# Kernel tuning notes

Hardware: AMD Instinct MI355X
Metric: run time of the kernel (lower is better)

## Reference

```python
import jax, jax.numpy as jnp
import numpy as np

B, N, D, H = 8, 2048, 256, 4
HD = D // H


def setup_inputs() -> dict:
    key = jax.random.key(0)
    ks = jax.random.split(key, 12)
    s = 1.0 / np.sqrt(D)
    inp = {
        "node_features": jax.random.normal(ks[0], (B, N, D), dtype=jnp.float32),
        "causal_mask": jnp.tril(jnp.ones((N, N), dtype=jnp.float32)),
        "Wq": jax.random.normal(ks[1], (D, D), dtype=jnp.float32) * s,
        "bq": jnp.zeros((D,), dtype=jnp.float32),
        "Wk": jax.random.normal(ks[2], (D, D), dtype=jnp.float32) * s,
        "bk": jnp.zeros((D,), dtype=jnp.float32),
        "Wv": jax.random.normal(ks[3], (D, D), dtype=jnp.float32) * s,
        "bv": jnp.zeros((D,), dtype=jnp.float32),
        "Wo": jax.random.normal(ks[4], (D, D), dtype=jnp.float32) * s,
        "bo": jnp.zeros((D,), dtype=jnp.float32),
        "Wu": jax.random.normal(ks[5], (2 * D, D), dtype=jnp.float32) * (1.0 / np.sqrt(2 * D)),
        "bu": jnp.zeros((D,), dtype=jnp.float32),
    }
    return inp


def reference(node_features, causal_mask, Wq, bq, Wk, bk, Wv, bv, Wo, bo, Wu, bu):
    # node_features: [B, N, D]; causal_mask: [N, N] (1 = keep, 0 = masked)
    x = node_features
    # project and split heads -> [B, H, N, HD]
    def heads(w, b):
        return (x @ w + b).reshape(B, N, H, HD).transpose(0, 2, 1, 3)
    q, k, v = heads(Wq, bq), heads(Wk, bk), heads(Wv, bv)
    scale = 1.0 / np.sqrt(HD).astype(np.float32)
    scores = jnp.einsum("bhnd,bhmd->bhnm", q, k) * scale  # [B, H, N, N]
    scores = jnp.where(causal_mask > 0, scores, jnp.float32(-1e9))
    attn = jax.nn.softmax(scores, axis=-1)
    ctx = jnp.einsum("bhnm,bhmd->bhnd", attn, v)  # [B, H, N, HD]
    messages = ctx.transpose(0, 2, 1, 3).reshape(B, N, D) @ Wo + bo  # [B, N, D]
    combined = jnp.concatenate([x, messages], axis=-1)  # [B, N, 2D]
    updated = jax.nn.relu(combined @ Wu + bu)  # [B, N, D]  (dropout = identity in eval)
    return updated
```

## Files before the change

kernel.cpp:

```cpp
#include <hip/hip_runtime.h>
#include <math.h>

constexpr int B  = 8;
constexpr int N  = 2048;
constexpr int D  = 256;
constexpr int H  = 4;
constexpr int HD = 64;
constexpr int MTOT = B * N;

typedef __attribute__((ext_vector_type(8))) short  short8;
typedef __attribute__((ext_vector_type(4))) float  floatx4;
typedef unsigned short ushort_t;

#define QSCALE 0.1803368801111204f

__device__ __forceinline__ unsigned short f2bf(float f) {
    unsigned u = __float_as_uint(f);
    u += 0x7fffu + ((u >> 16) & 1u);
    return (unsigned short)(u >> 16);
}

__device__ __forceinline__ unsigned short f2bf_t(float f) {
    return (unsigned short)(__float_as_uint(f) >> 16);
}

__device__ __forceinline__ void gl_lds16(const ushort_t* g, ushort_t* l) {
    __builtin_amdgcn_global_load_lds(
        (const __attribute__((address_space(1))) void*)g,
        (__attribute__((address_space(3))) void*)l, 16, 0, 0);
}

__global__ __launch_bounds__(256) void prep(
    const float* __restrict__ x,
    const float* __restrict__ Wq, const float* __restrict__ Wk,
    const float* __restrict__ Wv, const float* __restrict__ Wo,
    const float* __restrict__ Wu,
    ushort_t* __restrict__ xb,
    ushort_t* __restrict__ wqkvt, ushort_t* __restrict__ wut,
    ushort_t* __restrict__ wbt,   ushort_t* __restrict__ wob)
{
    __shared__ float Ls[64][65];
    const int bx = blockIdx.x;
    const int t  = threadIdx.x;

    if (bx < 2048) {
        int idx = (bx * 256 + t) * 8;
        float4 a = *(const float4*)(x + idx);
        float4 b = *(const float4*)(x + idx + 4);
        ushort_t o[8] = {f2bf(a.x), f2bf(a.y), f2bf(a.z), f2bf(a.w),
                         f2bf(b.x), f2bf(b.y), f2bf(b.z), f2bf(b.w)};
        *(short8*)(xb + idx) = *(const short8*)o;
        return;
    }

    if (bx < 2112) {
        const int e  = bx - 2048;
        const int zz = e >> 4;
        const int kt = (e >> 2) & 3;
        const int nt = e & 3;
        const float* src; ushort_t* dst; int K;
        if      (zz == 0) { src = Wq; dst = wqkvt;          K = 256; }
        else if (zz == 1) { src = Wk; dst = wqkvt + 65536;  K = 256; }
        else if (zz == 2) { src = Wv; dst = wqkvt + 131072; K = 256; }
        else              { src = Wu; dst = wut;            K = 512; }
        #pragma unroll
        for (int i = 0; i < 16; i++) {
            int ee = t + i * 256, r = ee >> 6, c = ee & 63;
            Ls[r][c] = src[(size_t)(kt * 64 + r) * 256 + nt * 64 + c];
        }
        __syncthreads();
        #pragma unroll
        for (int i = 0; i < 16; i++) {
            int ee = t + i * 256, r = ee >> 6, c = ee & 63;
            dst[(size_t)(nt * 64 + r) * K + kt * 64 + c] = f2bf(Ls[c][r]);
        }
        return;
    }

    if (bx < 2128) {
        const int e  = bx - 2112;
        const int kt = e >> 2;
        const int nt = e & 3;
        #pragma unroll
        for (int i = 0; i < 16; i++) {
            int ee = t + i * 256, r = ee >> 6, c = ee & 63;
            Ls[r][c] = Wu[(size_t)(256 + kt * 64 + r) * 256 + nt * 64 + c];
        }
        __syncthreads();
        #pragma unroll
        for (int i = 0; i < 16; i++) {
            int ee = t + i * 256, r = ee >> 6, c = ee & 63;
            wbt[(size_t)(nt * 64 + r) * 256 + kt * 64 + c] = f2bf(Ls[c][r]);
        }
        return;
    }

    {
        int idx = ((bx - 2128) * 256 + t) * 8;
        float4 a = *(const float4*)(Wo + idx);
        float4 b = *(const float4*)(Wo + idx + 4);
        ushort_t o[8] = {f2bf(a.x), f2bf(a.y), f2bf(a.z), f2bf(a.w),
                         f2bf(b.x), f2bf(b.y), f2bf(b.z), f2bf(b.w)};
        *(short8*)(wob + idx) = *(const short8*)o;
    }
}

__global__ __launch_bounds__(256) void qkv_gemm(
    const ushort_t* __restrict__ xb, const ushort_t* __restrict__ wqkvt,
    const ushort_t* __restrict__ wob, const ushort_t* __restrict__ wbt,
    const float* __restrict__ Wu,
    const float* __restrict__ bq, const float* __restrict__ bk,
    const float* __restrict__ bv, const float* __restrict__ bo,
    const float* __restrict__ bu,
    ushort_t* __restrict__ q, ushort_t* __restrict__ kout,
    ushort_t* __restrict__ vt,
    ushort_t* __restrict__ wut, float* __restrict__ b2)
{
    __shared__ ushort_t SH[16896];
    ushort_t* As = SH;
    ushort_t* Bs = SH + 8192;

    const int t = threadIdx.x, w = t >> 6, lane = t & 63;
    const int quad = lane >> 4, l16 = lane & 15;
    const int bx = blockIdx.x;
    const int wr = (w >> 1) * 64, wc = (w & 1) * 64;

    if (blockIdx.y == 128) {
        if (bx < 4) {
            const int row0 = (bx >> 1) * 128;
            const int col0 = (bx & 1) * 128;
            floatx4 acc[4][4] = {};
            for (int k0 = 0; k0 < 256; k0 += 64) {
                __syncthreads();
                #pragma unroll
                for (int i = 0; i < 4; i++) {
                    int e = t + (i << 8);
                    int r = e >> 3, c8 = (e & 7) << 3;
                    gl_lds16(wob + (size_t)(row0 + r) * 256 + k0 + c8, &As[e * 8]);
                    gl_lds16(wbt + (size_t)(col0 + r) * 256 + k0 + c8, &Bs[e * 8]);
                }
                __syncthreads();
                #pragma unroll
                for (int kk = 0; kk < 64; kk += 32) {
                    short8 af[4], bf[4];
                    #pragma unroll
                    for (int i = 0; i < 4; i++)
                        af[i] = *(const short8*)&As[(wr + i * 16 + l16) * 64 + kk + quad * 8];
                    #pragma unroll
                    for (int j = 0; j < 4; j++)
                        bf[j] = *(const short8*)&Bs[(wc + j * 16 + l16) * 64 + kk + quad * 8];
                    #pragma unroll
                    for (int i = 0; i < 4; i++)
                        #pragma unroll
                        for (int j = 0; j < 4; j++)
                            acc[i][j] = __builtin_amdgcn_mfma_f32_16x16x32_bf16(
                                af[i], bf[j], acc[i][j], 0, 0, 0);
                }
            }
            #pragma unroll
            for (int j = 0; j < 4; j++) {
                int cl = wc + j * 16 + l16;
                #pragma unroll
                for (int i = 0; i < 4; i++)
                    #pragma unroll
                    for (int r = 0; r < 4; r++) {
                        int ml = wr + i * 16 + quad * 4 + r;
                        wut[(size_t)(col0 + cl) * 512 + 256 + row0 + ml] =
                            f2bf(acc[i][j][r]);
                    }
            }
        } else if (bx == 4) {
            float s0 = 0.f, s1 = 0.f, s2 = 0.f, s3 = 0.f;
            for (int j = 0; j < 64; j++) {
                s0 = fmaf(bo[j],       Wu[(size_t)(256 + j)       * 256 + t], s0);
                s1 = fmaf(bo[j + 64],  Wu[(size_t)(256 + j + 64)  * 256 + t], s1);
                s2 = fmaf(bo[j + 128], Wu[(size_t)(256 + j + 128) * 256 + t], s2);
                s3 = fmaf(bo[j + 192], Wu[(size_t)(256 + j + 192) * 256 + t], s3);
            }
            b2[t] = bu[t] + ((s0 + s1) + (s2 + s3));
        }
        return;
    }

    const int col0 = bx * 128, row0 = blockIdx.y * 128;

    floatx4 acc[4][4] = {};

    for (int k0 = 0; k0 < 256; k0 += 64) {
        __syncthreads();
        #pragma unroll
        for (int i = 0; i < 4; i++) {
            int e = t + (i << 8);
            int r = e >> 3, c8 = (e & 7) << 3;
            gl_lds16(xb    + (size_t)(row0 + r) * 256 + k0 + c8, &As[e * 8]);
            gl_lds16(wqkvt + (size_t)(col0 + r) * 256 + k0 + c8, &Bs[e * 8]);
        }
        __syncthreads();

        #pragma unroll
        for (int kk = 0; kk < 64; kk += 32) {
            short8 af[4], bf[4];
            #pragma unroll
            for (int i = 0; i < 4; i++)
                af[i] = *(const short8*)&As[(wr + i * 16 + l16) * 64 + kk + quad * 8];
            #pragma unroll
            for (int j = 0; j < 4; j++)
                bf[j] = *(const short8*)&Bs[(wc + j * 16 + l16) * 64 + kk + quad * 8];
            #pragma unroll
            for (int i = 0; i < 4; i++)
                #pragma unroll
                for (int j = 0; j < 4; j++)
                    acc[i][j] = __builtin_amdgcn_mfma_f32_16x16x32_bf16(
                        af[i], bf[j], acc[i][j], 0, 0, 0);
        }
    }

    const int kind = bx >> 1;
    const float* bias = (kind == 0) ? bq : (kind == 1 ? bk : bv);
    const float scl  = (kind == 0) ? QSCALE : 1.0f;
    __syncthreads();
    ushort_t (*Ts)[132] = (ushort_t(*)[132])SH;
    #pragma unroll
    for (int j = 0; j < 4; j++) {
        int cl = wc + j * 16 + l16;
        float bsv = bias[(bx & 1) * 128 + cl];
        #pragma unroll
        for (int i = 0; i < 4; i++) {
            #pragma unroll
            for (int r = 0; r < 4; r++) {
                int ml = wr + i * 16 + quad * 4 + r;
                ushort_t bvv = f2bf((acc[i][j][r] + bsv) * scl);
                if (kind < 2) Ts[ml][cl] = bvv;
                else          Ts[cl][ml] = bvv;
            }
        }
    }
    __syncthreads();

    const int b = row0 >> 11, n0 = row0 & (N - 1);
    #pragma unroll
    for (int i = 0; i < 8; i++) {
        int id = t + (i << 8);
        int rr = id >> 4, c8 = (id & 15) << 3;
        short8 val = *(const short8*)&Ts[rr][c8];
        if (kind < 2) {
            int cg = (bx & 1) * 128 + c8;
            int h = cg >> 6, hd = cg & 63;
            if (kind == 0) {
                *(short8*)&q[(((size_t)(b * H + h)) * N + n0 + rr) * HD + hd] = val;
            } else {
                int hd2 = (((hd >> 3) ^ (rr & 7)) << 3);
                *(short8*)&kout[(((size_t)(b * H + h)) * N + n0 + rr) * HD + hd2] = val;
            }
        } else {
            int cg = (bx & 1) * 128 + rr;
            int h = cg >> 6, hd = cg & 63;
            int u  = id & 15;
            int up = (u & 8) | ((u ^ hd) & 7);
            *(short8*)&vt[(((size_t)(b * H + h)) * HD + hd) * N + n0 + (up << 3)] = val;
        }
    }
}

__global__ __launch_bounds__(512) void attn_mfma(
    const ushort_t* __restrict__ q,
    const ushort_t* __restrict__ k,
    const ushort_t* __restrict__ vt,
    ushort_t* __restrict__ ctxb)
{
    __shared__ ushort_t Ks [2][128 * 64];
    __shared__ ushort_t Vts[2][64 * 128];
    __shared__ ushort_t Ps [8][16][36];

    const int t    = threadIdx.x;
    const int w    = t >> 6;
    const int lane = t & 63;
    const int quad = lane >> 4;
    const int l16  = lane & 15;
    const int swz  = l16 & 7;
    const int bh   = blockIdx.x;
    const int b    = bh >> 2, h = bh & 3;
    const int by   = blockIdx.y;
    const int grp  = w >> 2;
    const int qt   = grp ? by : (31 - by);
    const int qbase = qt * 64;
    const int rowb  = qbase + (w & 3) * 16;

    const ushort_t* qp = q  + (size_t)bh * N * HD;
    const ushort_t* kp = k  + (size_t)bh * N * HD;
    const ushort_t* vp = vt + (size_t)bh * HD * N;

    short8 qf0, qf1;
    {
        const ushort_t* qrow = qp + (size_t)(rowb + l16) * HD + quad * 8;
        qf0 = *(const short8*)(qrow);
        qf1 = *(const short8*)(qrow + 32);
    }

    floatx4 acc_o[4] = {};
    float plsum[4] = {};

    const int nkt_self = (qt >> 1) + 1;
    const int nkt_max  = ((31 - by) >> 1) + 1;

    #pragma unroll
    for (int i = 0; i < 2; i++) {
        int e = t + (i << 9);
        gl_lds16(kp + (((size_t)(e >> 3)) << 6) + ((e & 7) << 3),
                 &Ks[0][e * 8]);
        gl_lds16(vp + (size_t)(e >> 4) * N + ((e & 15) << 3),
                 &Vts[0][e * 8]);
    }
    __syncthreads();

    for (int kt = 0; kt < nkt_max; kt++) {
        const int kbase = kt * 128;
        const int cur   = kt & 1;

        if (kt + 1 < nkt_max) {
            const int kb2 = kbase + 128;
            #pragma unroll
            for (int i = 0; i < 2; i++) {
                int e = t + (i << 9);
                gl_lds16(kp + (((size_t)(kb2 + (e >> 3))) << 6) + ((e & 7) << 3),
                         &Ks[cur ^ 1][e * 8]);
                gl_lds16(vp + (size_t)(e >> 4) * N + kb2 + ((e & 15) << 3),
                         &Vts[cur ^ 1][e * 8]);
            }
        }

        if (kt < nkt_self) {
            const ushort_t* Ksc  = Ks[cur];
            const ushort_t* Vtsc = Vts[cur];

            int rem = rowb + 15 - kbase;
            int nch = (rem < 0) ? 0 : ((rem >> 5) + 1);
            if (nch > 4) nch = 4;

            for (int ch = 0; ch < nch; ch++) {
                #pragma unroll
                for (int c2 = 0; c2 < 2; c2++) {
                    const int ct = ch * 2 + c2;
                    const int krow = (ct * 16 + l16) * 64;
                    short8 kf0 = *(const short8*)&Ksc[krow + ((quad ^ swz) << 3)];
                    short8 kf1 = *(const short8*)&Ksc[krow + (((4 + quad) ^ swz) << 3)];
                    floatx4 z = {0.0f, 0.0f, 0.0f, 0.0f};
                    __builtin_amdgcn_s_setprio(1);
                    floatx4 s = __builtin_amdgcn_mfma_f32_16x16x32_bf16(qf0, kf0, z, 0, 0, 0);
                    s         = __builtin_amdgcn_mfma_f32_16x16x32_bf16(qf1, kf1, s, 0, 0, 0);
                    __builtin_amdgcn_s_setprio(0);
                    const bool partial = (kbase + ct * 16 + 15) > rowb;
                    if (partial) {
                        const int keyg = kbase + ct * 16 + l16;
                        #pragma unroll
                        for (int r = 0; r < 4; r++) {
                            float sv = s[r];
                            if (keyg > rowb + quad * 4 + r) sv = -3.0e38f;
                            float pv = __builtin_amdgcn_exp2f(sv);
                            plsum[r] += pv;
                            Ps[w][quad * 4 + r][c2 * 16 + l16] = f2bf_t(pv);
                        }
                    } else {
                        #pragma unroll
                        for (int r = 0; r < 4; r++) {
                            float pv = __builtin_amdgcn_exp2f(s[r]);
                            plsum[r] += pv;
                            Ps[w][quad * 4 + r][c2 * 16 + l16] = f2bf_t(pv);
                        }
                    }
                }
                short8 pf = *(const short8*)&Ps[w][l16][quad * 8];
                const int uu = ch * 4 + quad;
                const int up = (uu & 8) | ((uu ^ l16) & 7);
                __builtin_amdgcn_s_setprio(1);
                #pragma unroll
                for (int nt = 0; nt < 4; nt++) {
                    short8 vf = *(const short8*)&Vtsc[(nt * 16 + l16) * 128 + (up << 3)];
                    acc_o[nt] = __builtin_amdgcn_mfma_f32_16x16x32_bf16(pf, vf, acc_o[nt], 0, 0, 0);
                }
                __builtin_amdgcn_s_setprio(0);
            }
        }

        __syncthreads();
    }

    #pragma unroll
    for (int r = 0; r < 4; r++) {
        float l = plsum[r];
        l += __shfl_xor(l, 1);
        l += __shfl_xor(l, 2);
        l += __shfl_xor(l, 4);
        l += __shfl_xor(l, 8);
        float inv = 1.0f / l;
        int   n   = rowb + quad * 4 + r;
        #pragma unroll
        for (int nt = 0; nt < 4; nt++) {
            ctxb[((size_t)(b * N + n)) * D + h * HD + nt * 16 + l16] =
                f2bf(acc_o[nt][r] * inv);
        }
    }
}

__global__ __launch_bounds__(256) void tail2(
    const ushort_t* __restrict__ xb, const ushort_t* __restrict__ ctxb,
    const ushort_t* __restrict__ wut, const float* __restrict__ b2,
    float* __restrict__ out)
{
    __shared__ ushort_t As[64 * 64];
    __shared__ ushort_t Bs[128 * 64];

    const int t = threadIdx.x, w = t >> 6, lane = t & 63;
    const int quad = lane >> 4, l16 = lane & 15;
    const int col0 = blockIdx.x * 128, row0 = blockIdx.y * 64;
    const int wr = (w >> 1) * 32, wc = (w & 1) * 64;

    floatx4 acc[2][4] = {};

    for (int k0 = 0; k0 < 512; k0 += 64) {
        const ushort_t* Ab = (k0 < 256) ? xb : ctxb;
        const int ka = k0 & 255;
        __syncthreads();
        #pragma unroll
        for (int i = 0; i < 2; i++) {
            int e = t + (i << 8);
            int r = e >> 3, c8 = (e & 7) << 3;
            gl_lds16(Ab + (size_t)(row0 + r) * 256 + ka + c8, &As[e * 8]);
        }
        #pragma unroll
        for (int i = 0; i < 4; i++) {
            int e = t + (i << 8);
            int r = e >> 3, c8 = (e & 7) << 3;
            gl_lds16(wut + (size_t)(col0 + r) * 512 + k0 + c8, &Bs[e * 8]);
        }
        __syncthreads();

        #pragma unroll
        for (int kk = 0; kk < 64; kk += 32) {
            short8 af[2], bf[4];
            #pragma unroll
            for (int i = 0; i < 2; i++)
                af[i] = *(const short8*)&As[(wr + i * 16 + l16) * 64 + kk + quad * 8];
            #pragma unroll
            for (int j = 0; j < 4; j++)
                bf[j] = *(const short8*)&Bs[(wc + j * 16 + l16) * 64 + kk + quad * 8];
            #pragma unroll
            for (int i = 0; i < 2; i++)
                #pragma unroll
                for (int j = 0; j < 4; j++)
                    acc[i][j] = __builtin_amdgcn_mfma_f32_16x16x32_bf16(
                        af[i], bf[j], acc[i][j], 0, 0, 0);
        }
    }

    #pragma unroll
    for (int j = 0; j < 4; j++) {
        int col = col0 + wc + j * 16 + l16;
        float bsv = b2[col];
        #pragma unroll
        for (int i = 0; i < 2; i++) {
            #pragma unroll
            for (int r = 0; r < 4; r++) {
                int m = row0 + wr + i * 16 + quad * 4 + r;
                out[(size_t)m * 256 + col] = fmaxf(acc[i][j][r] + bsv, 0.0f);
            }
        }
    }
}

extern "C" void kernel_launch(void* const* d_in, const int* in_sizes, int n_in,
                              void* d_out, int out_size, void* d_ws, size_t ws_size,
                              hipStream_t stream)
{
    const float* x  = (const float*)d_in[0];
    const float* Wq = (const float*)d_in[2];
    const float* bq = (const float*)d_in[3];
    const float* Wk = (const float*)d_in[4];
    const float* bk = (const float*)d_in[5];
    const float* Wv = (const float*)d_in[6];
    const float* bv = (const float*)d_in[7];
    const float* Wo = (const float*)d_in[8];
    const float* bo = (const float*)d_in[9];
    const float* Wu = (const float*)d_in[10];
    const float* bu = (const float*)d_in[11];
    float* out = (float*)d_out;

    const size_t SZ = (size_t)MTOT * D;
    ushort_t* xb    = (ushort_t*)d_ws;
    ushort_t* qb    = xb    + SZ;
    ushort_t* kb    = qb    + SZ;
    ushort_t* vbt   = kb    + SZ;
    ushort_t* ctxb  = vbt   + SZ;
    ushort_t* wqkvt = ctxb  + SZ;
    ushort_t* wut   = wqkvt + 196608;
    ushort_t* wbt   = wut   + 131072;
    ushort_t* wob   = wbt   + 65536;
    float*    b2    = (float*)(wob + 65536);

    prep<<<2160, 256, 0, stream>>>(x, Wq, Wk, Wv, Wo, Wu,
                                   xb, wqkvt, wut, wbt, wob);

    qkv_gemm<<<dim3(6, 129), 256, 0, stream>>>(
        xb, wqkvt, wob, wbt, Wu, bq, bk, bv, bo, bu,
        qb, kb, vbt, wut, b2);

    attn_mfma<<<dim3(32, 16), 512, 0, stream>>>(qb, kb, vbt, ctxb);

    tail2<<<dim3(2, 256), 256, 0, stream>>>(xb, ctxb, wut, b2, out);
}
```

Baseline: 167.5 us.

## Double-buffer LDS tiles in QKV and output GEMMs to overlap loads with MFMA

The QKV projection GEMM, the fused weight precompute GEMM and the tail output GEMM now keep two LDS buffers. Each step prefetches the next K-slice with global-to-LDS loads while the current slice is fed to MFMAs, which cuts one barrier per iteration. MFMA sections are wrapped in s_setprio so that waves doing math get scheduling priority. LDS use per block doubles (64KB for qkv_gemm), which can lower occupancy.

```diff
diff --git a/kernel.cpp b/kernel.cpp
--- a/kernel.cpp
+++ b/kernel.cpp
@@ -116,9 +116,9 @@
     ushort_t* __restrict__ vt,
     ushort_t* __restrict__ wut, float* __restrict__ b2)
 {
-    __shared__ ushort_t SH[16896];
-    ushort_t* As = SH;
-    ushort_t* Bs = SH + 8192;
+    __shared__ ushort_t SH[32768];
+    ushort_t* Asb[2] = { SH,         SH + 8192  };
+    ushort_t* Bsb[2] = { SH + 16384, SH + 24576 };
 
     const int t = threadIdx.x, w = t >> 6, lane = t & 63;
     const int quad = lane >> 4, l16 = lane & 15;
@@ -130,32 +130,47 @@
             const int row0 = (bx >> 1) * 128;
             const int col0 = (bx & 1) * 128;
             floatx4 acc[4][4] = {};
-            for (int k0 = 0; k0 < 256; k0 += 64) {
-                __syncthreads();
-                #pragma unroll
-                for (int i = 0; i < 4; i++) {
-                    int e = t + (i << 8);
-                    int r = e >> 3, c8 = (e & 7) << 3;
-                    gl_lds16(wob + (size_t)(row0 + r) * 256 + k0 + c8, &As[e * 8]);
-                    gl_lds16(wbt + (size_t)(col0 + r) * 256 + k0 + c8, &Bs[e * 8]);
+            #pragma unroll
+            for (int i = 0; i < 4; i++) {
+                int e = t + (i << 8);
+                int r = e >> 3, c8 = (e & 7) << 3;
+                gl_lds16(wob + (size_t)(row0 + r) * 256 + c8, &Asb[0][e * 8]);
+                gl_lds16(wbt + (size_t)(col0 + r) * 256 + c8, &Bsb[0][e * 8]);
+            }
+            __syncthreads();
+            for (int ks = 0; ks < 4; ks++) {
+                const int cur = ks & 1;
+                if (ks < 3) {
+                    const int k0n = (ks + 1) * 64;
+                    #pragma unroll
+                    for (int i = 0; i < 4; i++) {
+                        int e = t + (i << 8);
+                        int r = e >> 3, c8 = (e & 7) << 3;
+                        gl_lds16(wob + (size_t)(row0 + r) * 256 + k0n + c8,
+                                 &Asb[cur ^ 1][e * 8]);
+                        gl_lds16(wbt + (size_t)(col0 + r) * 256 + k0n + c8,
+                                 &Bsb[cur ^ 1][e * 8]);
+                    }
                 }
-                __syncthreads();
                 #pragma unroll
                 for (int kk = 0; kk < 64; kk += 32) {
                     short8 af[4], bf[4];
                     #pragma unroll
                     for (int i = 0; i < 4; i++)
-                        af[i] = *(const short8*)&As[(wr + i * 16 + l16) * 64 + kk + quad * 8];
+                        af[i] = *(const short8*)&Asb[cur][(wr + i * 16 + l16) * 64 + kk + quad * 8];
                     #pragma unroll
                     for (int j = 0; j < 4; j++)
-                        bf[j] = *(const short8*)&Bs[(wc + j * 16 + l16) * 64 + kk + quad * 8];
+                        bf[j] = *(const short8*)&Bsb[cur][(wc + j * 16 + l16) * 64 + kk + quad * 8];
+                    __builtin_amdgcn_s_setprio(1);
                     #pragma unroll
                     for (int i = 0; i < 4; i++)
                         #pragma unroll
                         for (int j = 0; j < 4; j++)
                             acc[i][j] = __builtin_amdgcn_mfma_f32_16x16x32_bf16(
                                 af[i], bf[j], acc[i][j], 0, 0, 0);
+                    __builtin_amdgcn_s_setprio(0);
                 }
+                __syncthreads();
             }
             #pragma unroll
             for (int j = 0; j < 4; j++) {
@@ -186,39 +201,54 @@
 
     floatx4 acc[4][4] = {};
 
-    for (int k0 = 0; k0 < 256; k0 += 64) {
-        __syncthreads();
-        #pragma unroll
-        for (int i = 0; i < 4; i++) {
-            int e = t + (i << 8);
-            int r = e >> 3, c8 = (e & 7) << 3;
-            gl_lds16(xb    + (size_t)(row0 + r) * 256 + k0 + c8, &As[e * 8]);
-            gl_lds16(wqkvt + (size_t)(col0 + r) * 256 + k0 + c8, &Bs[e * 8]);
-        }
-        __syncthreads();
+    #pragma unroll
+    for (int i = 0; i < 4; i++) {
+        int e = t + (i << 8);
+        int r = e >> 3, c8 = (e & 7) << 3;
+        gl_lds16(xb    + (size_t)(row0 + r) * 256 + c8, &Asb[0][e * 8]);
+        gl_lds16(wqkvt + (size_t)(col0 + r) * 256 + c8, &Bsb[0][e * 8]);
+    }
+    __syncthreads();
+
+    for (int ks = 0; ks < 4; ks++) {
+        const int cur = ks & 1;
+        if (ks < 3) {
+            const int k0n = (ks + 1) * 64;
+            #pragma unroll
+            for (int i = 0; i < 4; i++) {
+                int e = t + (i << 8);
+                int r = e >> 3, c8 = (e & 7) << 3;
+                gl_lds16(xb    + (size_t)(row0 + r) * 256 + k0n + c8,
+                         &Asb[cur ^ 1][e * 8]);
+                gl_lds16(wqkvt + (size_t)(col0 + r) * 256 + k0n + c8,
+                         &Bsb[cur ^ 1][e * 8]);
+            }
+        }
 
         #pragma unroll
         for (int kk = 0; kk < 64; kk += 32) {
             short8 af[4], bf[4];
             #pragma unroll
             for (int i = 0; i < 4; i++)
-                af[i] = *(const short8*)&As[(wr + i * 16 + l16) * 64 + kk + quad * 8];
+                af[i] = *(const short8*)&Asb[cur][(wr + i * 16 + l16) * 64 + kk + quad * 8];
             #pragma unroll
             for (int j = 0; j < 4; j++)
-                bf[j] = *(const short8*)&Bs[(wc + j * 16 + l16) * 64 + kk + quad * 8];
+                bf[j] = *(const short8*)&Bsb[cur][(wc + j * 16 + l16) * 64 + kk + quad * 8];
+            __builtin_amdgcn_s_setprio(1);
             #pragma unroll
             for (int i = 0; i < 4; i++)
                 #pragma unroll
                 for (int j = 0; j < 4; j++)
                     acc[i][j] = __builtin_amdgcn_mfma_f32_16x16x32_bf16(
                         af[i], bf[j], acc[i][j], 0, 0, 0);
-        }
+            __builtin_amdgcn_s_setprio(0);
+        }
+        __syncthreads();
     }
 
     const int kind = bx >> 1;
     const float* bias = (kind == 0) ? bq : (kind == 1 ? bk : bv);
     const float scl  = (kind == 0) ? QSCALE : 1.0f;
-    __syncthreads();
     ushort_t (*Ts)[132] = (ushort_t(*)[132])SH;
     #pragma unroll
     for (int j = 0; j < 4; j++) {
@@ -407,8 +437,8 @@
     const ushort_t* __restrict__ wut, const float* __restrict__ b2,
     float* __restrict__ out)
 {
-    __shared__ ushort_t As[64 * 64];
-    __shared__ ushort_t Bs[128 * 64];
+    __shared__ ushort_t As[2][64 * 64];
+    __shared__ ushort_t Bs[2][128 * 64];
 
     const int t = threadIdx.x, w = t >> 6, lane = t & 63;
     const int quad = lane >> 4, l16 = lane & 15;
@@ -417,40 +447,61 @@
 
     floatx4 acc[2][4] = {};
 
-    for (int k0 = 0; k0 < 512; k0 += 64) {
-        const ushort_t* Ab = (k0 < 256) ? xb : ctxb;
-        const int ka = k0 & 255;
-        __syncthreads();
-        #pragma unroll
-        for (int i = 0; i < 2; i++) {
-            int e = t + (i << 8);
-            int r = e >> 3, c8 = (e & 7) << 3;
-            gl_lds16(Ab + (size_t)(row0 + r) * 256 + ka + c8, &As[e * 8]);
-        }
-        #pragma unroll
-        for (int i = 0; i < 4; i++) {
-            int e = t + (i << 8);
-            int r = e >> 3, c8 = (e & 7) << 3;
-            gl_lds16(wut + (size_t)(col0 + r) * 512 + k0 + c8, &Bs[e * 8]);
-        }
-        __syncthreads();
+    #pragma unroll
+    for (int i = 0; i < 2; i++) {
+        int e = t + (i << 8);
+        int r = e >> 3, c8 = (e & 7) << 3;
+        gl_lds16(xb + (size_t)(row0 + r) * 256 + c8, &As[0][e * 8]);
+    }
+    #pragma unroll
+    for (int i = 0; i < 4; i++) {
+        int e = t + (i << 8);
+        int r = e >> 3, c8 = (e & 7) << 3;
+        gl_lds16(wut + (size_t)(col0 + r) * 512 + c8, &Bs[0][e * 8]);
+    }
+    __syncthreads();
+
+    for (int ks = 0; ks < 8; ks++) {
+        const int cur = ks & 1;
+        if (ks < 7) {
+            const int k0n = (ks + 1) * 64;
+            const ushort_t* Ab = (k0n < 256) ? xb : ctxb;
+            const int ka = k0n & 255;
+            #pragma unroll
+            for (int i = 0; i < 2; i++) {
+                int e = t + (i << 8);
+                int r = e >> 3, c8 = (e & 7) << 3;
+                gl_lds16(Ab + (size_t)(row0 + r) * 256 + ka + c8,
+                         &As[cur ^ 1][e * 8]);
+            }
+            #pragma unroll
+            for (int i = 0; i < 4; i++) {
+                int e = t + (i << 8);
+                int r = e >> 3, c8 = (e & 7) << 3;
+                gl_lds16(wut + (size_t)(col0 + r) * 512 + k0n + c8,
+                         &Bs[cur ^ 1][e * 8]);
+            }
+        }
 
         #pragma unroll
         for (int kk = 0; kk < 64; kk += 32) {
             short8 af[2], bf[4];
             #pragma unroll
             for (int i = 0; i < 2; i++)
-                af[i] = *(const short8*)&As[(wr + i * 16 + l16) * 64 + kk + quad * 8];
+                af[i] = *(const short8*)&As[cur][(wr + i * 16 + l16) * 64 + kk + quad * 8];
             #pragma unroll
             for (int j = 0; j < 4; j++)
-                bf[j] = *(const short8*)&Bs[(wc + j * 16 + l16) * 64 + kk + quad * 8];
+                bf[j] = *(const short8*)&Bs[cur][(wc + j * 16 + l16) * 64 + kk + quad * 8];
+            __builtin_amdgcn_s_setprio(1);
             #pragma unroll
             for (int i = 0; i < 2; i++)
                 #pragma unroll
                 for (int j = 0; j < 4; j++)
                     acc[i][j] = __builtin_amdgcn_mfma_f32_16x16x32_bf16(
                         af[i], bf[j], acc[i][j], 0, 0, 0);
-        }
+            __builtin_amdgcn_s_setprio(0);
+        }
+        __syncthreads();
     }
 
     #pragma unroll
```

Result: no change. 170.3 us (+1.7%).

## Load QKV GEMM fragments directly from global and double-buffer the tail GEMM

Applied to the files above, without the earlier changes.

The QKV projection and the Wo·Wu weight-fold GEMMs now read MFMA operand fragments straight from global memory into registers. This drops the LDS staging and the two barriers per K step, and fully unrolls the K loop. The tail GEMM gets double-buffered LDS tiles, so the next K slice is prefetched while the current one is multiplied, with one barrier per step. s_setprio is raised around MFMA blocks in both kernels. Direct global fragment loads are uncoalesced, 16-byte strided row reads, and rely on the L1/L2 caches for reuse across waves. They also raise register pressure.

```diff
diff --git a/kernel.cpp b/kernel.cpp
--- a/kernel.cpp
+++ b/kernel.cpp
@@ -116,9 +116,7 @@
     ushort_t* __restrict__ vt,
     ushort_t* __restrict__ wut, float* __restrict__ b2)
 {
-    __shared__ ushort_t SH[16896];
-    ushort_t* As = SH;
-    ushort_t* Bs = SH + 8192;
+    __shared__ ushort_t SH[128 * 132];
 
     const int t = threadIdx.x, w = t >> 6, lane = t & 63;
     const int quad = lane >> 4, l16 = lane & 15;
@@ -130,32 +128,25 @@
             const int row0 = (bx >> 1) * 128;
             const int col0 = (bx & 1) * 128;
             floatx4 acc[4][4] = {};
-            for (int k0 = 0; k0 < 256; k0 += 64) {
-                __syncthreads();
-                #pragma unroll
-                for (int i = 0; i < 4; i++) {
-                    int e = t + (i << 8);
-                    int r = e >> 3, c8 = (e & 7) << 3;
-                    gl_lds16(wob + (size_t)(row0 + r) * 256 + k0 + c8, &As[e * 8]);
-                    gl_lds16(wbt + (size_t)(col0 + r) * 256 + k0 + c8, &Bs[e * 8]);
-                }
-                __syncthreads();
-                #pragma unroll
-                for (int kk = 0; kk < 64; kk += 32) {
-                    short8 af[4], bf[4];
-                    #pragma unroll
-                    for (int i = 0; i < 4; i++)
-                        af[i] = *(const short8*)&As[(wr + i * 16 + l16) * 64 + kk + quad * 8];
+            const ushort_t* Arow = wob + (size_t)(row0 + wr + l16) * 256 + quad * 8;
+            const ushort_t* Brow = wbt + (size_t)(col0 + wc + l16) * 256 + quad * 8;
+            #pragma unroll
+            for (int k0 = 0; k0 < 256; k0 += 32) {
+                short8 af[4], bf[4];
+                #pragma unroll
+                for (int i = 0; i < 4; i++)
+                    af[i] = *(const short8*)(Arow + (size_t)i * 16 * 256 + k0);
+                #pragma unroll
+                for (int j = 0; j < 4; j++)
+                    bf[j] = *(const short8*)(Brow + (size_t)j * 16 * 256 + k0);
+                __builtin_amdgcn_s_setprio(1);
+                #pragma unroll
+                for (int i = 0; i < 4; i++)
                     #pragma unroll
                     for (int j = 0; j < 4; j++)
-                        bf[j] = *(const short8*)&Bs[(wc + j * 16 + l16) * 64 + kk + quad * 8];
-                    #pragma unroll
-                    for (int i = 0; i < 4; i++)
-                        #pragma unroll
-                        for (int j = 0; j < 4; j++)
-                            acc[i][j] = __builtin_amdgcn_mfma_f32_16x16x32_bf16(
-                                af[i], bf[j], acc[i][j], 0, 0, 0);
-                }
+                        acc[i][j] = __builtin_amdgcn_mfma_f32_16x16x32_bf16(
+                            af[i], bf[j], acc[i][j], 0, 0, 0);
+                __builtin_amdgcn_s_setprio(0);
             }
             #pragma unroll
             for (int j = 0; j < 4; j++) {
@@ -186,39 +177,30 @@
 
     floatx4 acc[4][4] = {};
 
-    for (int k0 = 0; k0 < 256; k0 += 64) {
-        __syncthreads();
-        #pragma unroll
-        for (int i = 0; i < 4; i++) {
-            int e = t + (i << 8);
-            int r = e >> 3, c8 = (e & 7) << 3;
-            gl_lds16(xb    + (size_t)(row0 + r) * 256 + k0 + c8, &As[e * 8]);
-            gl_lds16(wqkvt + (size_t)(col0 + r) * 256 + k0 + c8, &Bs[e * 8]);
-        }
-        __syncthreads();
-
-        #pragma unroll
-        for (int kk = 0; kk < 64; kk += 32) {
-            short8 af[4], bf[4];
-            #pragma unroll
-            for (int i = 0; i < 4; i++)
-                af[i] = *(const short8*)&As[(wr + i * 16 + l16) * 64 + kk + quad * 8];
+    const ushort_t* Arow = xb    + (size_t)(row0 + wr + l16) * 256 + quad * 8;
+    const ushort_t* Brow = wqkvt + (size_t)(col0 + wc + l16) * 256 + quad * 8;
+    #pragma unroll
+    for (int k0 = 0; k0 < 256; k0 += 32) {
+        short8 af[4], bf[4];
+        #pragma unroll
+        for (int i = 0; i < 4; i++)
+            af[i] = *(const short8*)(Arow + (size_t)i * 16 * 256 + k0);
+        #pragma unroll
+        for (int j = 0; j < 4; j++)
+            bf[j] = *(const short8*)(Brow + (size_t)j * 16 * 256 + k0);
+        __builtin_amdgcn_s_setprio(1);
+        #pragma unroll
+        for (int i = 0; i < 4; i++)
             #pragma unroll
             for (int j = 0; j < 4; j++)
-                bf[j] = *(const short8*)&Bs[(wc + j * 16 + l16) * 64 + kk + quad * 8];
-            #pragma unroll
-            for (int i = 0; i < 4; i++)
-                #pragma unroll
-                for (int j = 0; j < 4; j++)
-                    acc[i][j] = __builtin_amdgcn_mfma_f32_16x16x32_bf16(
-                        af[i], bf[j], acc[i][j], 0, 0, 0);
-        }
+                acc[i][j] = __builtin_amdgcn_mfma_f32_16x16x32_bf16(
+                    af[i], bf[j], acc[i][j], 0, 0, 0);
+        __builtin_amdgcn_s_setprio(0);
     }
 
     const int kind = bx >> 1;
     const float* bias = (kind == 0) ? bq : (kind == 1 ? bk : bv);
     const float scl  = (kind == 0) ? QSCALE : 1.0f;
-    __syncthreads();
     ushort_t (*Ts)[132] = (ushort_t(*)[132])SH;
     #pragma unroll
     for (int j = 0; j < 4; j++) {
@@ -407,8 +389,8 @@
     const ushort_t* __restrict__ wut, const float* __restrict__ b2,
     float* __restrict__ out)
 {
-    __shared__ ushort_t As[64 * 64];
-    __shared__ ushort_t Bs[128 * 64];
+    __shared__ ushort_t As[2][64 * 64];
+    __shared__ ushort_t Bs[2][128 * 64];
 
     const int t = threadIdx.x, w = t >> 6, lane = t & 63;
     const int quad = lane >> 4, l16 = lane & 15;
@@ -417,40 +399,61 @@
 
     floatx4 acc[2][4] = {};
 
-    for (int k0 = 0; k0 < 512; k0 += 64) {
-        const ushort_t* Ab = (k0 < 256) ? xb : ctxb;
-        const int ka = k0 & 255;
-        __syncthreads();
-        #pragma unroll
-        for (int i = 0; i < 2; i++) {
-            int e = t + (i << 8);
-            int r = e >> 3, c8 = (e & 7) << 3;
-            gl_lds16(Ab + (size_t)(row0 + r) * 256 + ka + c8, &As[e * 8]);
-        }
-        #pragma unroll
-        for (int i = 0; i < 4; i++) {
-            int e = t + (i << 8);
-            int r = e >> 3, c8 = (e & 7) << 3;
-            gl_lds16(wut + (size_t)(col0 + r) * 512 + k0 + c8, &Bs[e * 8]);
-        }
-        __syncthreads();
+    #pragma unroll
+    for (int i = 0; i < 2; i++) {
+        int e = t + (i << 8);
+        int r = e >> 3, c8 = (e & 7) << 3;
+        gl_lds16(xb + (size_t)(row0 + r) * 256 + c8, &As[0][e * 8]);
+    }
+    #pragma unroll
+    for (int i = 0; i < 4; i++) {
+        int e = t + (i << 8);
+        int r = e >> 3, c8 = (e & 7) << 3;
+        gl_lds16(wut + (size_t)(col0 + r) * 512 + c8, &Bs[0][e * 8]);
+    }
+    __syncthreads();
+
+    for (int ks = 0; ks < 8; ks++) {
+        const int cur = ks & 1;
+        if (ks < 7) {
+            const int k0n = (ks + 1) * 64;
+            const ushort_t* Ab = (k0n < 256) ? xb : ctxb;
+            const int ka = k0n & 255;
+            #pragma unroll
+            for (int i = 0; i < 2; i++) {
+                int e = t + (i << 8);
+                int r = e >> 3, c8 = (e & 7) << 3;
+                gl_lds16(Ab + (size_t)(row0 + r) * 256 + ka + c8,
+                         &As[cur ^ 1][e * 8]);
+            }
+            #pragma unroll
+            for (int i = 0; i < 4; i++) {
+                int e = t + (i << 8);
+                int r = e >> 3, c8 = (e & 7) << 3;
+                gl_lds16(wut + (size_t)(col0 + r) * 512 + k0n + c8,
+                         &Bs[cur ^ 1][e * 8]);
+            }
+        }
 
         #pragma unroll
         for (int kk = 0; kk < 64; kk += 32) {
             short8 af[2], bf[4];
             #pragma unroll
             for (int i = 0; i < 2; i++)
-                af[i] = *(const short8*)&As[(wr + i * 16 + l16) * 64 + kk + quad * 8];
+                af[i] = *(const short8*)&As[cur][(wr + i * 16 + l16) * 64 + kk + quad * 8];
             #pragma unroll
             for (int j = 0; j < 4; j++)
-                bf[j] = *(const short8*)&Bs[(wc + j * 16 + l16) * 64 + kk + quad * 8];
+                bf[j] = *(const short8*)&Bs[cur][(wc + j * 16 + l16) * 64 + kk + quad * 8];
+            __builtin_amdgcn_s_setprio(1);
             #pragma unroll
             for (int i = 0; i < 2; i++)
                 #pragma unroll
                 for (int j = 0; j < 4; j++)
                     acc[i][j] = __builtin_amdgcn_mfma_f32_16x16x32_bf16(
                         af[i], bf[j], acc[i][j], 0, 0, 0);
-        }
+            __builtin_amdgcn_s_setprio(0);
+        }
+        __syncthreads();
     }
 
     #pragma unroll
```

Measured after the change: 181.6 us. +8.4%, slower.
